# Kernel tuning notes

Measured on AMD Instinct MI355X. Metric: run time of the kernel, lower is better.

Reference implementation:

```python
import jax, jax.numpy as jnp
import numpy as np

_SAMPLING_EPS = 1e-05
_RMAX = 0.9999999403953552          # largest float32 uniform from tl.rand
_RMAX_LOG = -5.960464477539063e-08  # log(_RMAX)


def setup_inputs() -> dict:
    key = jax.random.key(0)
    k1, k2, k3, k4, k5 = jax.random.split(key, 5)
    B, V = 256, 128000
    logits = jax.random.normal(k1, (B, V), dtype=jnp.float32) * 4.0
    temperature = jax.random.uniform(k2, (B,), dtype=jnp.float32, minval=0.1, maxval=1.5)
    top_k = jax.random.randint(k3, (B,), 1, 1000).astype(jnp.int32)
    top_p = jax.random.uniform(k4, (B,), dtype=jnp.float32, minval=0.5, maxval=1.0)
    gumbel_u = jax.random.uniform(k5, (B, V), dtype=jnp.float32)
    return {
        "logits": logits,
        "temperature": temperature,
        "top_k": top_k,
        "top_p": top_p,
        "gumbel_u": gumbel_u,
        "num_logprobs": 20,
    }


def reference(logits, temperature, top_k, top_p, gumbel_u, num_logprobs):
    B, V = logits.shape
    # --- apply_temperature: divide by temp, temp<eps treated as 1.0 (greedy) ---
    temp = jnp.where(temperature < _SAMPLING_EPS, 1.0, temperature)
    logits = logits.astype(jnp.float32) / temp[:, None]

    # --- apply_top_k_top_p: sort ascending, mask, scatter back ---
    idx_sort = jnp.argsort(logits, axis=-1)                      # ascending
    logits_sort = jnp.take_along_axis(logits, idx_sort, axis=-1)
    # top-k: value of the k-th largest is at position V-k in ascending order
    k_pos = (V - top_k.astype(jnp.int32))[:, None]
    thresh = jnp.take_along_axis(logits_sort, k_pos, axis=-1)    # [B,1]
    logits_sort = jnp.where(logits_sort < thresh, -jnp.inf, logits_sort)
    # top-p: drop ascending prefix whose cumulative prob <= 1-p (keep last)
    probs_sort = jax.nn.softmax(logits_sort, axis=-1)
    cum = jnp.cumsum(probs_sort, axis=-1)
    mask_p = cum <= (1.0 - top_p)[:, None]
    mask_p = mask_p.at[:, -1].set(False)
    logits_sort = jnp.where(mask_p, -jnp.inf, logits_sort)
    # unsort back to vocab order
    inv = jnp.argsort(idx_sort, axis=-1)
    logits_f = jnp.take_along_axis(logits_sort, inv, axis=-1)

    # --- softmax + gumbel-trick sampling: argmax(p / -log(u)) ---
    probs = jax.nn.softmax(logits_f, axis=-1)
    q = -jnp.where(gumbel_u >= _RMAX, _RMAX_LOG, jnp.log(gumbel_u))
    greedy = (temperature < _SAMPLING_EPS)[:, None]  # kernel skips these rows
    ratio = jnp.where(greedy, probs, probs / q)
    sampled = jnp.argmax(ratio, axis=-1)             # [B]

    # --- gather_logprobs ---
    logprobs = jax.nn.log_softmax(logits_f, axis=-1)
    sampled_lp = jnp.take_along_axis(logprobs, sampled[:, None], axis=-1)  # [B,1]
    ranks = jnp.sum(logprobs > sampled_lp, axis=-1)                        # [B]
    topk_lp, topk_idx = jax.lax.top_k(logprobs, num_logprobs)
    indices = jnp.concatenate([sampled[:, None], topk_idx], axis=1)        # [B,1+K]
    lp_vals = jnp.concatenate([sampled_lp, topk_lp], axis=1)               # [B,1+K]

    return sampled[:, None], indices, lp_vals, ranks
```

## Files before the change

### kernel.cpp

```cpp
#include <hip/hip_runtime.h>
#include <math.h>

#define NTHR 1024
#define CAP 4096
#define BINS 4096

#define RMAX_F 0.9999999403953552f
#define RMAX_LOG_F -5.960464477539063e-08f
#define NEG_BIG -3.0e38f

__device__ __forceinline__ unsigned keyOf(float v) {
    unsigned b = __float_as_uint(v);
    return (b & 0x80000000u) ? ~b : (b | 0x80000000u);
}
__device__ __forceinline__ float valOfKey(unsigned k) {
    unsigned b = (k & 0x80000000u) ? (k ^ 0x80000000u) : ~k;
    return __uint_as_float(b);
}

__global__ __launch_bounds__(NTHR) void sampler_kernel(
    const float* __restrict__ logits,
    const float* __restrict__ temperature,
    const int* __restrict__ top_kv,
    const float* __restrict__ top_pv,
    const float* __restrict__ gumbel,
    float* __restrict__ out,
    int B, int V, int K)
{
    const int r = blockIdx.x;
    const int tid = threadIdx.x;
    const int lane = tid & 63;

    __shared__ unsigned long long cand[CAP];
    __shared__ int scanI[NTHR];
    __shared__ float varr[1024];
    __shared__ float Earr[1024];
    __shared__ float sfx[1024];
    __shared__ unsigned char flagArr[1024];
    __shared__ unsigned bitmap[64];
    __shared__ unsigned s_prefix;
    __shared__ int s_cntgt, s_total, s_lvl;
    __shared__ int s_ncand, s_nkeep, s_rank, s_g0, s_g1;
    __shared__ unsigned long long s_amax;
    __shared__ float s_vs;

    unsigned* hist = (unsigned*)cand;

    const float* row = logits + (long long)r * V;
    const float* urow = gumbel + (long long)r * V;

    float traw = temperature[r];
    bool greedy = traw < 1e-5f;
    float t = greedy ? 1.0f : traw;
    int k = top_kv[r];
    if (k < 1) k = 1;
    if (k > V) k = V;
    float p = top_pv[r];

    const float4* row4 = (const float4*)row;
    const int V4 = V >> 2;
    const int Vt = V4 << 2;
    const unsigned cpy = tid & 1u;

    for (int i = tid; i < BINS * 2; i += NTHR) hist[i] = 0;
    __syncthreads();
    for (int i = tid; i < V4; i += NTHR) {
        float4 l4 = row4[i];
        unsigned k0 = keyOf(l4.x), k1 = keyOf(l4.y), k2 = keyOf(l4.z), k3 = keyOf(l4.w);
        atomicAdd(&hist[((k0 >> 20) << 1) | cpy], 1u);
        atomicAdd(&hist[((k1 >> 20) << 1) | cpy], 1u);
        atomicAdd(&hist[((k2 >> 20) << 1) | cpy], 1u);
        atomicAdd(&hist[((k3 >> 20) << 1) | cpy], 1u);
    }
    for (int i = Vt + tid; i < V; i += NTHR) {
        unsigned key = keyOf(row[i]);
        atomicAdd(&hist[((key >> 20) << 1) | cpy], 1u);
    }
    __syncthreads();
    {
        int base = tid << 2;
        int cs = 0;
        #pragma unroll
        for (int j = 0; j < 4; ++j)
            cs += (int)(hist[(base + j) * 2] + hist[(base + j) * 2 + 1]);
        scanI[tid] = cs;
    }
    __syncthreads();
    for (int d = 1; d < NTHR; d <<= 1) {
        int v = (tid + d < NTHR) ? scanI[tid + d] : 0;
        __syncthreads();
        scanI[tid] += v;
        __syncthreads();
    }
    {
        int mine = scanI[tid];
        int above = (tid + 1 < NTHR) ? scanI[tid + 1] : 0;
        if (mine >= k && above < k) {
            int base = tid << 2;
            int run = above;
            for (int b = base + 3; b >= base; --b) {
                int mb = (int)(hist[b * 2] + hist[b * 2 + 1]);
                if (run + mb >= k) {
                    s_prefix = (unsigned)b; s_cntgt = run; s_total = run + mb; s_lvl = 0;
                    break;
                }
                run += mb;
            }
        }
    }
    for (int level = 1; level <= 2; ++level) {
        __syncthreads();
        if (s_total <= CAP) break;
        for (int i = tid; i < 512; i += NTHR) hist[i] = 0;
        __syncthreads();
        unsigned pfx = s_prefix;
        const int msh = 32 - (12 + 8 * (level - 1));
        const int bsh = msh - 8;
        for (int i = tid; i < V4; i += NTHR) {
            float4 l4 = row4[i];
            float vv[4] = { l4.x, l4.y, l4.z, l4.w };
            #pragma unroll
            for (int j = 0; j < 4; ++j) {
                unsigned key = keyOf(vv[j]);
                if ((key >> msh) == pfx)
                    atomicAdd(&hist[(((key >> bsh) & 255u) << 1) | cpy], 1u);
            }
        }
        for (int i = Vt + tid; i < V; i += NTHR) {
            unsigned key = keyOf(row[i]);
            if ((key >> msh) == pfx)
                atomicAdd(&hist[(((key >> bsh) & 255u) << 1) | cpy], 1u);
        }
        __syncthreads();
        if (tid == 0) {
            int run = s_cntgt;
            for (int b = 255; b >= 0; --b) {
                int mb = (int)(hist[b * 2] + hist[b * 2 + 1]);
                if (run + mb >= k) {
                    s_prefix = (pfx << 8) | (unsigned)b; s_cntgt = run; s_total = run + mb;
                    break;
                }
                run += mb;
            }
            s_lvl = level;
        }
    }
    __syncthreads();
    const unsigned tlo = s_prefix << (20 - 8 * s_lvl);
    if (tid == 0) s_ncand = 0;
    __syncthreads();

    for (int i = tid; i < V4; i += NTHR) {
        float4 l4 = row4[i];
        float vv[4] = { l4.x, l4.y, l4.z, l4.w };
        #pragma unroll
        for (int j = 0; j < 4; ++j) {
            unsigned key = keyOf(vv[j]);
            bool pred = (key >= tlo);
            unsigned long long mask = __ballot(pred ? 1 : 0);
            if (mask) {
                int leader = __ffsll(mask) - 1;
                int cnt = __popcll(mask);
                int base = 0;
                if (lane == leader) base = atomicAdd(&s_ncand, cnt);
                base = __shfl(base, leader);
                if (pred) {
                    int pos = base + __popcll(mask & ((1ULL << lane) - 1ULL));
                    if (pos < CAP) {
                        unsigned gidx = (unsigned)(i * 4 + j);
                        cand[pos] = ((unsigned long long)key << 32) | (unsigned)(~gidx);
                    }
                }
            }
        }
    }
    for (int i = Vt + tid; i < V; i += NTHR) {
        unsigned key = keyOf(row[i]);
        bool pred = (key >= tlo);
        unsigned long long mask = __ballot(pred ? 1 : 0);
        if (mask) {
            int leader = __ffsll(mask) - 1;
            int cnt = __popcll(mask);
            int base = 0;
            if (lane == leader) base = atomicAdd(&s_ncand, cnt);
            base = __shfl(base, leader);
            if (pred) {
                int pos = base + __popcll(mask & ((1ULL << lane) - 1ULL));
                if (pos < CAP) {
                    unsigned gidx = (unsigned)i;
                    cand[pos] = ((unsigned long long)key << 32) | (unsigned)(~gidx);
                }
            }
        }
    }
    __syncthreads();
    int ncand = s_ncand; if (ncand > CAP) ncand = CAP;
    if (k > ncand) k = ncand;

    int P = 2; while (P < ncand) P <<= 1;
    for (int i = ncand + tid; i < P; i += NTHR) cand[i] = 0ULL;
    __syncthreads();
    for (int size = 2; size <= P; size <<= 1) {
        for (int stride = size >> 1; stride > 0; stride >>= 1) {
            for (int i = tid; i < P; i += NTHR) {
                int j = i ^ stride;
                if (j > i) {
                    unsigned long long a = cand[i], b = cand[j];
                    bool up = ((i & size) == 0);
                    bool sw = up ? (a < b) : (a > b);
                    if (sw) { cand[i] = b; cand[j] = a; }
                }
            }
            __syncthreads();
        }
    }

    for (int i = tid; i < 1024; i += NTHR)
        varr[i] = (i < ncand) ? (valOfKey((unsigned)(cand[i] >> 32)) / t) : NEG_BIG;
    __syncthreads();

    const float m = varr[0];
    const float tkeyV = varr[k - 1];
    int ntop = k;
    while (ntop < ncand) {
        float vi = (ntop < 1024) ? varr[ntop]
                                 : (valOfKey((unsigned)(cand[ntop] >> 32)) / t);
        if (vi != tkeyV) break;
        ++ntop;
    }
    if (ntop > 1024) ntop = 1024;

    for (int i = tid; i < 1024; i += NTHR) {
        float e = (i < ntop) ? expf(varr[i] - m) : 0.0f;
        Earr[i] = e;
        sfx[i] = e;
    }
    __syncthreads();
    for (int d = 1; d < 1024; d <<= 1) {
        float t0 = (tid + d < 1024) ? sfx[tid + d] : 0.0f;
        __syncthreads();
        sfx[tid] += t0;
        __syncthreads();
    }
    const float Zp = sfx[0];
    const float cmp = 1.0f - p;
    if (tid == 0) { s_nkeep = 0; s_rank = 0; s_amax = 0ULL; }
    for (int i = tid; i < 64; i += NTHR) bitmap[i] = 0;
    __syncthreads();
    {
        int local = 0;
        for (int i = tid; i < ntop; i += NTHR)
            if (sfx[i] / Zp > cmp) local++;
        if (local) atomicAdd(&s_nkeep, local);
    }
    __syncthreads();
    const int nkeep = s_nkeep;
    if (tid == 0) {
        float vb = varr[nkeep - 1];
        int g0 = nkeep - 1;
        while (g0 > 0 && varr[g0 - 1] == vb) --g0;
        int g1 = nkeep;
        while (g1 < ntop && varr[g1] == vb) ++g1;
        s_g0 = g0; s_g1 = g1;
    }
    __syncthreads();
    const int g0 = s_g0, g1 = s_g1;
    const int mkeep = nkeep - g0;
    for (int i = g0 + tid; i < g1; i += NTHR) {
        unsigned gi = ~(unsigned)(cand[i] & 0xFFFFFFFFull);
        int rk = 0;
        for (int j = g0; j < g1; ++j) {
            unsigned gj = ~(unsigned)(cand[j] & 0xFFFFFFFFull);
            if (gj > gi) rk++;
        }
        flagArr[i] = (rk < mkeep) ? 1 : 0;
    }
    __syncthreads();

    const float Z2 = (nkeep < 1024) ? (Zp - sfx[nkeep]) : Zp;
    const float L = logf(Z2);

    for (int i = tid; i < g1; i += NTHR) {
        if (i < g0 || flagArr[i]) {
            unsigned lo = (unsigned)(cand[i] & 0xFFFFFFFFull);
            unsigned gidx = ~lo;
            float u = urow[gidx];
            float q = -((u >= RMAX_F) ? RMAX_LOG_F : logf(u));
            float prob = Earr[i] / Z2;
            float ratio = greedy ? prob : (prob / q);
            unsigned long long comp = ((unsigned long long)__float_as_uint(ratio) << 32) | lo;
            atomicMax(&s_amax, comp);
            if (gidx < 2048) atomicOr(&bitmap[gidx >> 5], 1u << (gidx & 31));
        }
    }
    __syncthreads();
    const unsigned samp_lo = (unsigned)(s_amax & 0xFFFFFFFFull);
    const unsigned samp = ~samp_lo;
    for (int i = tid; i < ntop; i += NTHR)
        if ((unsigned)(cand[i] & 0xFFFFFFFFull) == samp_lo) s_vs = varr[i];
    __syncthreads();
    const float lp_s = (s_vs - m) - L;
    {
        int local = 0;
        for (int i = tid; i < nkeep; i += NTHR)
            if ((varr[i] - m) - L > lp_s) local++;
        if (local) atomicAdd(&s_rank, local);
    }
    __syncthreads();

    if (tid == 0) {
        float* o_samp = out;
        float* o_idx  = out + B;
        float* o_lp   = out + B + (long long)B * (K + 1);
        float* o_rank = out + B + 2LL * B * (K + 1);
        long long rowo = (long long)r * (K + 1);

        o_samp[r] = (float)samp;
        o_idx[rowo] = (float)samp;
        o_lp[rowo] = lp_s;
        o_rank[r] = (float)s_rank;

        int ntk = (nkeep < K) ? nkeep : K;
        int slot = 0, i = 0;
        while (slot < ntk && i < g1) {
            float v = varr[i];
            int re = i + 1;
            while (re < g1 && varr[re] == v) ++re;
            long long last = -1;
            while (slot < ntk) {
                unsigned best = 0xFFFFFFFFu;
                for (int j = i; j < re; ++j) {
                    if (j >= g0 && !flagArr[j]) continue;
                    unsigned gj = ~(unsigned)(cand[j] & 0xFFFFFFFFull);
                    if ((long long)gj > last && gj < best) best = gj;
                }
                if (best == 0xFFFFFFFFu) break;
                o_idx[rowo + 1 + slot] = (float)best;
                o_lp[rowo + 1 + slot] = (v - m) - L;
                last = best; ++slot;
            }
            i = re;
        }
        if (nkeep < K) {
            int j = 0;
            for (int c = nkeep; c < K; ++c) {
                while (bitmap[j >> 5] & (1u << (j & 31))) ++j;
                o_idx[rowo + 1 + c] = (float)j;
                o_lp[rowo + 1 + c] = NEG_BIG;
                ++j;
            }
        }
    }
}

extern "C" void kernel_launch(void* const* d_in, const int* in_sizes, int n_in,
                              void* d_out, int out_size, void* d_ws, size_t ws_size,
                              hipStream_t stream) {
    const float* logits      = (const float*)d_in[0];
    const float* temperature = (const float*)d_in[1];
    const int*   top_k       = (const int*)d_in[2];
    const float* top_p       = (const float*)d_in[3];
    const float* gumbel      = (const float*)d_in[4];
    int B = in_sizes[1];
    int V = in_sizes[0] / B;
    int K = (out_size / B - 4) / 2;
    sampler_kernel<<<B, NTHR, 0, stream>>>(logits, temperature, top_k, top_p,
                                           gumbel, (float*)d_out, B, V, K);
}
```

Measured before the change: 317.1 us.

## Refine candidate threshold, register bitonic sort, warp-level scans and reductions

Unrolls the histogram and candidate-collection passes to issue four float4 loads per iteration. Replaces the shared-memory Hillis-Steele scan with wave shuffle scans. When more than 1024 candidates survive, a refinement histogram over the candidates narrows the threshold so the sort runs in registers with shuffles for strides below 64. Argmax, keep-count and rank reductions now use wave shuffles before the shared atomics, and the serial top-K output loop on thread 0 is replaced by parallel per-thread slot computation. The changes add code complexity, and the guard-band refinement is a risk for threshold-tie correctness.

```diff
diff --git a/kernel.cpp b/kernel.cpp
--- a/kernel.cpp
+++ b/kernel.cpp
@@ -4,6 +4,8 @@
 #define NTHR 1024
 #define CAP 4096
 #define BINS 4096
+#define SMALL 1024
+#define GUARD 16u
 
 #define RMAX_F 0.9999999403953552f
 #define RMAX_LOG_F -5.960464477539063e-08f
@@ -16,6 +18,11 @@
 __device__ __forceinline__ float valOfKey(unsigned k) {
     unsigned b = (k & 0x80000000u) ? (k ^ 0x80000000u) : ~k;
     return __uint_as_float(b);
+}
+__device__ __forceinline__ unsigned long long shflXor64(unsigned long long v, int m) {
+    int lo = __shfl_xor((int)(unsigned)v, m);
+    int hi = __shfl_xor((int)(unsigned)(v >> 32), m);
+    return ((unsigned long long)(unsigned)hi << 32) | (unsigned)lo;
 }
 
 __global__ __launch_bounds__(NTHR) void sampler_kernel(
@@ -30,9 +37,12 @@
     const int r = blockIdx.x;
     const int tid = threadIdx.x;
     const int lane = tid & 63;
+    const int wid = tid >> 6;
 
     __shared__ unsigned long long cand[CAP];
-    __shared__ int scanI[NTHR];
+    __shared__ unsigned long long cand2[SMALL];
+    __shared__ unsigned refHist[512];
+    __shared__ int wtotI[16];
     __shared__ float varr[1024];
     __shared__ float Earr[1024];
     __shared__ float sfx[1024];
@@ -40,7 +50,7 @@
     __shared__ unsigned bitmap[64];
     __shared__ unsigned s_prefix;
     __shared__ int s_cntgt, s_total, s_lvl;
-    __shared__ int s_ncand, s_nkeep, s_rank, s_g0, s_g1;
+    __shared__ int s_ncand, s_nc2, s_nkeep, s_rank, s_g0, s_g1;
     __shared__ unsigned long long s_amax;
     __shared__ float s_vs;
 
@@ -64,17 +74,27 @@
 
     for (int i = tid; i < BINS * 2; i += NTHR) hist[i] = 0;
     __syncthreads();
-    for (int i = tid; i < V4; i += NTHR) {
-        float4 l4 = row4[i];
-        unsigned k0 = keyOf(l4.x), k1 = keyOf(l4.y), k2 = keyOf(l4.z), k3 = keyOf(l4.w);
-        atomicAdd(&hist[((k0 >> 20) << 1) | cpy], 1u);
-        atomicAdd(&hist[((k1 >> 20) << 1) | cpy], 1u);
-        atomicAdd(&hist[((k2 >> 20) << 1) | cpy], 1u);
-        atomicAdd(&hist[((k3 >> 20) << 1) | cpy], 1u);
-    }
-    for (int i = Vt + tid; i < V; i += NTHR) {
-        unsigned key = keyOf(row[i]);
-        atomicAdd(&hist[((key >> 20) << 1) | cpy], 1u);
+#define H4(v4) do { \
+        atomicAdd(&hist[((keyOf((v4).x) >> 20) << 1) | cpy], 1u); \
+        atomicAdd(&hist[((keyOf((v4).y) >> 20) << 1) | cpy], 1u); \
+        atomicAdd(&hist[((keyOf((v4).z) >> 20) << 1) | cpy], 1u); \
+        atomicAdd(&hist[((keyOf((v4).w) >> 20) << 1) | cpy], 1u); \
+    } while (0)
+    {
+        int i = tid;
+        for (; i + 3 * NTHR < V4; i += 4 * NTHR) {
+            float4 a = row4[i];
+            float4 b = row4[i + NTHR];
+            float4 c = row4[i + 2 * NTHR];
+            float4 d = row4[i + 3 * NTHR];
+            H4(a); H4(b); H4(c); H4(d);
+        }
+        for (; i < V4; i += NTHR) {
+            float4 a = row4[i];
+            H4(a);
+        }
+        for (int ii = Vt + tid; ii < V; ii += NTHR)
+            atomicAdd(&hist[((keyOf(row[ii]) >> 20) << 1) | cpy], 1u);
     }
     __syncthreads();
     {
@@ -83,20 +103,19 @@
         #pragma unroll
         for (int j = 0; j < 4; ++j)
             cs += (int)(hist[(base + j) * 2] + hist[(base + j) * 2 + 1]);
-        scanI[tid] = cs;
-    }
-    __syncthreads();
-    for (int d = 1; d < NTHR; d <<= 1) {
-        int v = (tid + d < NTHR) ? scanI[tid + d] : 0;
-        __syncthreads();
-        scanI[tid] += v;
-        __syncthreads();
-    }
-    {
-        int mine = scanI[tid];
-        int above = (tid + 1 < NTHR) ? scanI[tid + 1] : 0;
+        int vv = cs;
+        #pragma unroll
+        for (int d = 1; d < 64; d <<= 1) {
+            int o = __shfl_down(vv, d);
+            if (lane + d < 64) vv += o;
+        }
+        if (lane == 0) wtotI[wid] = vv;
+        __syncthreads();
+        int off = 0;
+        for (int w = wid + 1; w < 16; ++w) off += wtotI[w];
+        int mine = vv + off;
+        int above = mine - cs;
         if (mine >= k && above < k) {
-            int base = tid << 2;
             int run = above;
             for (int b = base + 3; b >= base; --b) {
                 int mb = (int)(hist[b * 2] + hist[b * 2 + 1]);
@@ -147,77 +166,173 @@
     }
     __syncthreads();
     const unsigned tlo = s_prefix << (20 - 8 * s_lvl);
+    const float thrF = valOfKey(tlo);
     if (tid == 0) s_ncand = 0;
     __syncthreads();
 
-    for (int i = tid; i < V4; i += NTHR) {
-        float4 l4 = row4[i];
-        float vv[4] = { l4.x, l4.y, l4.z, l4.w };
-        #pragma unroll
-        for (int j = 0; j < 4; ++j) {
-            unsigned key = keyOf(vv[j]);
-            bool pred = (key >= tlo);
+#define EMIT_CAND(val, gidx_) do { \
+        bool pred = ((val) >= thrF); \
+        unsigned long long mask = __ballot(pred ? 1 : 0); \
+        if (mask) { \
+            int leader = __ffsll(mask) - 1; \
+            int cnt = __popcll(mask); \
+            int bpos = 0; \
+            if (lane == leader) bpos = atomicAdd(&s_ncand, cnt); \
+            bpos = __shfl(bpos, leader); \
+            if (pred) { \
+                int pos = bpos + __popcll(mask & ((1ULL << lane) - 1ULL)); \
+                if (pos < CAP) { \
+                    unsigned key = keyOf(val); \
+                    cand[pos] = ((unsigned long long)key << 32) | (unsigned)(~(gidx_)); \
+                } \
+            } \
+        } \
+    } while (0)
+#define C4(v4, i4) do { \
+        EMIT_CAND((v4).x, (unsigned)((i4) * 4 + 0)); \
+        EMIT_CAND((v4).y, (unsigned)((i4) * 4 + 1)); \
+        EMIT_CAND((v4).z, (unsigned)((i4) * 4 + 2)); \
+        EMIT_CAND((v4).w, (unsigned)((i4) * 4 + 3)); \
+    } while (0)
+    {
+        int i = tid;
+        for (; i + 3 * NTHR < V4; i += 4 * NTHR) {
+            float4 a = row4[i];
+            float4 b = row4[i + NTHR];
+            float4 c = row4[i + 2 * NTHR];
+            float4 d = row4[i + 3 * NTHR];
+            C4(a, i); C4(b, i + NTHR); C4(c, i + 2 * NTHR); C4(d, i + 3 * NTHR);
+        }
+        for (; i < V4; i += NTHR) {
+            float4 a = row4[i];
+            C4(a, i);
+        }
+        for (int ii = Vt + tid; ii < V; ii += NTHR) {
+            float lv = row[ii];
+            EMIT_CAND(lv, (unsigned)ii);
+        }
+    }
+    __syncthreads();
+    int ncand = s_ncand; if (ncand > CAP) ncand = CAP;
+    if (k > ncand) k = ncand;
+
+    bool fromC2 = false;
+    bool bigSort = false;
+    if (ncand > SMALL) {
+        unsigned pfx = s_prefix;
+        int run = s_cntgt;
+        int bb = 20 - 8 * s_lvl;
+        while (bb > 0) {
+            int step = (bb >= 8) ? 8 : bb;
+            bb -= step;
+            int nbins = 1 << step;
+            for (int i = tid; i < nbins * 2; i += NTHR) refHist[i] = 0;
+            __syncthreads();
+            for (int i = tid; i < ncand; i += NTHR) {
+                unsigned key = (unsigned)(cand[i] >> 32);
+                if ((key >> (bb + step)) == pfx)
+                    atomicAdd(&refHist[(((key >> bb) & (unsigned)(nbins - 1)) << 1) | cpy], 1u);
+            }
+            __syncthreads();
+            int cnt = 0;
+            if (tid < 256) cnt = (tid < nbins) ? (int)(refHist[tid * 2] + refHist[tid * 2 + 1]) : 0;
+            int vv = cnt;
+            #pragma unroll
+            for (int d = 1; d < 64; d <<= 1) {
+                int o = __shfl_down(vv, d);
+                if (lane + d < 64) vv += o;
+            }
+            if (tid < 256 && lane == 0) wtotI[wid] = vv;
+            __syncthreads();
+            if (tid < 256) {
+                int off = 0;
+                for (int w = wid + 1; w < 4; ++w) off += wtotI[w];
+                int incl = vv + off;
+                int abv = incl - cnt;
+                int kk = k - run;
+                if (incl >= kk && abv < kk) {
+                    s_prefix = (pfx << step) | (unsigned)tid;
+                    s_cntgt = run + abv;
+                }
+            }
+            __syncthreads();
+            pfx = s_prefix;
+            run = s_cntgt;
+        }
+        unsigned tref = (pfx >= tlo + GUARD) ? (pfx - GUARD) : tlo;
+        if (tid == 0) s_nc2 = 0;
+        __syncthreads();
+        for (int i = tid; i < ncand; i += NTHR) {
+            unsigned long long cv = cand[i];
+            bool pred = ((unsigned)(cv >> 32) >= tref);
             unsigned long long mask = __ballot(pred ? 1 : 0);
             if (mask) {
                 int leader = __ffsll(mask) - 1;
-                int cnt = __popcll(mask);
-                int base = 0;
-                if (lane == leader) base = atomicAdd(&s_ncand, cnt);
-                base = __shfl(base, leader);
+                int cnt2 = __popcll(mask);
+                int bpos = 0;
+                if (lane == leader) bpos = atomicAdd(&s_nc2, cnt2);
+                bpos = __shfl(bpos, leader);
                 if (pred) {
-                    int pos = base + __popcll(mask & ((1ULL << lane) - 1ULL));
-                    if (pos < CAP) {
-                        unsigned gidx = (unsigned)(i * 4 + j);
-                        cand[pos] = ((unsigned long long)key << 32) | (unsigned)(~gidx);
+                    int pos = bpos + __popcll(mask & ((1ULL << lane) - 1ULL));
+                    if (pos < SMALL) cand2[pos] = cv;
+                }
+            }
+        }
+        __syncthreads();
+        int nc2 = s_nc2;
+        if (nc2 <= SMALL) { ncand = nc2; fromC2 = true; }
+        else bigSort = true;
+    }
+
+    unsigned long long vreg = 0ULL;
+    if (!bigSort) {
+        const unsigned long long* src = fromC2 ? cand2 : cand;
+        unsigned long long v = (tid < ncand) ? src[tid] : 0ULL;
+        #pragma unroll
+        for (int size = 2; size <= SMALL; size <<= 1) {
+            #pragma unroll
+            for (int stride = size >> 1; stride > 0; stride >>= 1) {
+                unsigned long long o;
+                if (stride < 64) {
+                    o = shflXor64(v, stride);
+                } else {
+                    cand[tid] = v;
+                    __syncthreads();
+                    o = cand[tid ^ stride];
+                    __syncthreads();
+                }
+                bool takeMax = (((tid & size) == 0) == ((tid & stride) == 0));
+                unsigned long long mx = (v > o) ? v : o;
+                unsigned long long mn = (v > o) ? o : v;
+                v = takeMax ? mx : mn;
+            }
+        }
+        cand[tid] = v;
+        vreg = v;
+        varr[tid] = (tid < ncand) ? (valOfKey((unsigned)(vreg >> 32)) / t) : NEG_BIG;
+        __syncthreads();
+    } else {
+        int P = 2; while (P < ncand) P <<= 1;
+        for (int i = ncand + tid; i < P; i += NTHR) cand[i] = 0ULL;
+        __syncthreads();
+        for (int size = 2; size <= P; size <<= 1) {
+            for (int stride = size >> 1; stride > 0; stride >>= 1) {
+                for (int i = tid; i < P; i += NTHR) {
+                    int j = i ^ stride;
+                    if (j > i) {
+                        unsigned long long a = cand[i], b = cand[j];
+                        bool up = ((i & size) == 0);
+                        bool sw = up ? (a < b) : (a > b);
+                        if (sw) { cand[i] = b; cand[j] = a; }
                     }
                 }
-            }
-        }
-    }
-    for (int i = Vt + tid; i < V; i += NTHR) {
-        unsigned key = keyOf(row[i]);
-        bool pred = (key >= tlo);
-        unsigned long long mask = __ballot(pred ? 1 : 0);
-        if (mask) {
-            int leader = __ffsll(mask) - 1;
-            int cnt = __popcll(mask);
-            int base = 0;
-            if (lane == leader) base = atomicAdd(&s_ncand, cnt);
-            base = __shfl(base, leader);
-            if (pred) {
-                int pos = base + __popcll(mask & ((1ULL << lane) - 1ULL));
-                if (pos < CAP) {
-                    unsigned gidx = (unsigned)i;
-                    cand[pos] = ((unsigned long long)key << 32) | (unsigned)(~gidx);
-                }
-            }
-        }
-    }
-    __syncthreads();
-    int ncand = s_ncand; if (ncand > CAP) ncand = CAP;
-    if (k > ncand) k = ncand;
-
-    int P = 2; while (P < ncand) P <<= 1;
-    for (int i = ncand + tid; i < P; i += NTHR) cand[i] = 0ULL;
-    __syncthreads();
-    for (int size = 2; size <= P; size <<= 1) {
-        for (int stride = size >> 1; stride > 0; stride >>= 1) {
-            for (int i = tid; i < P; i += NTHR) {
-                int j = i ^ stride;
-                if (j > i) {
-                    unsigned long long a = cand[i], b = cand[j];
-                    bool up = ((i & size) == 0);
-                    bool sw = up ? (a < b) : (a > b);
-                    if (sw) { cand[i] = b; cand[j] = a; }
-                }
-            }
-            __syncthreads();
-        }
-    }
-
-    for (int i = tid; i < 1024; i += NTHR)
-        varr[i] = (i < ncand) ? (valOfKey((unsigned)(cand[i] >> 32)) / t) : NEG_BIG;
-    __syncthreads();
+                __syncthreads();
+            }
+        }
+        for (int i = tid; i < 1024; i += NTHR)
+            varr[i] = (i < ncand) ? (valOfKey((unsigned)(cand[i] >> 32)) / t) : NEG_BIG;
+        __syncthreads();
+    }
 
     const float m = varr[0];
     const float tkeyV = varr[k - 1];
@@ -230,10 +345,10 @@
     }
     if (ntop > 1024) ntop = 1024;
 
-    for (int i = tid; i < 1024; i += NTHR) {
-        float e = (i < ntop) ? expf(varr[i] - m) : 0.0f;
-        Earr[i] = e;
-        sfx[i] = e;
+    {
+        float e = (tid < ntop) ? expf(varr[tid] - m) : 0.0f;
+        Earr[tid] = e;
+        sfx[tid] = e;
     }
     __syncthreads();
     for (int d = 1; d < 1024; d <<= 1) {
@@ -251,7 +366,9 @@
         int local = 0;
         for (int i = tid; i < ntop; i += NTHR)
             if (sfx[i] / Zp > cmp) local++;
-        if (local) atomicAdd(&s_nkeep, local);
+        #pragma unroll
+        for (int d = 1; d < 64; d <<= 1) local += __shfl_xor(local, d);
+        if (lane == 0 && local) atomicAdd(&s_nkeep, local);
     }
     __syncthreads();
     const int nkeep = s_nkeep;
@@ -280,18 +397,27 @@
     const float Z2 = (nkeep < 1024) ? (Zp - sfx[nkeep]) : Zp;
     const float L = logf(Z2);
 
-    for (int i = tid; i < g1; i += NTHR) {
-        if (i < g0 || flagArr[i]) {
-            unsigned lo = (unsigned)(cand[i] & 0xFFFFFFFFull);
-            unsigned gidx = ~lo;
-            float u = urow[gidx];
-            float q = -((u >= RMAX_F) ? RMAX_LOG_F : logf(u));
-            float prob = Earr[i] / Z2;
-            float ratio = greedy ? prob : (prob / q);
-            unsigned long long comp = ((unsigned long long)__float_as_uint(ratio) << 32) | lo;
-            atomicMax(&s_amax, comp);
-            if (gidx < 2048) atomicOr(&bitmap[gidx >> 5], 1u << (gidx & 31));
-        }
+    {
+        unsigned long long lm = 0ULL;
+        for (int i = tid; i < g1; i += NTHR) {
+            if (i < g0 || flagArr[i]) {
+                unsigned lo = (unsigned)(cand[i] & 0xFFFFFFFFull);
+                unsigned gidx = ~lo;
+                float u = urow[gidx];
+                float q = -((u >= RMAX_F) ? RMAX_LOG_F : logf(u));
+                float prob = Earr[i] / Z2;
+                float ratio = greedy ? prob : (prob / q);
+                unsigned long long comp = ((unsigned long long)__float_as_uint(ratio) << 32) | lo;
+                if (comp > lm) lm = comp;
+                if (gidx < 2048) atomicOr(&bitmap[gidx >> 5], 1u << (gidx & 31));
+            }
+        }
+        #pragma unroll
+        for (int d = 1; d < 64; d <<= 1) {
+            unsigned long long o = shflXor64(lm, d);
+            if (o > lm) lm = o;
+        }
+        if (lane == 0 && lm) atomicMax(&s_amax, lm);
     }
     __syncthreads();
     const unsigned samp_lo = (unsigned)(s_amax & 0xFFFFFFFFull);
@@ -304,43 +430,54 @@
         int local = 0;
         for (int i = tid; i < nkeep; i += NTHR)
             if ((varr[i] - m) - L > lp_s) local++;
-        if (local) atomicAdd(&s_rank, local);
-    }
-    __syncthreads();
+        #pragma unroll
+        for (int d = 1; d < 64; d <<= 1) local += __shfl_xor(local, d);
+        if (lane == 0 && local) atomicAdd(&s_rank, local);
+    }
+    __syncthreads();
+
+    float* o_samp = out;
+    float* o_idx  = out + B;
+    float* o_lp   = out + B + (long long)B * (K + 1);
+    float* o_rank = out + B + 2LL * B * (K + 1);
+    const long long rowo = (long long)r * (K + 1);
+    const int ntk = (nkeep < K) ? nkeep : K;
+
+    if (tid < g1) {
+        const int i = tid;
+        bool kept = (i < g0) || flagArr[i];
+        if (kept) {
+            float v = varr[i];
+            int rs, re, base;
+            if (i >= g0) { rs = g0; re = g1; base = g0; }
+            else {
+                rs = i; while (rs > 0 && varr[rs - 1] == v) --rs;
+                re = i + 1; while (re < g1 && varr[re] == v) ++re;
+                base = rs;
+            }
+            if (base < ntk) {
+                unsigned myidx = ~(unsigned)(cand[i] & 0xFFFFFFFFull);
+                int cnt = 0;
+                for (int j = rs; j < re; ++j) {
+                    if (j == i) continue;
+                    if (j >= g0 && !flagArr[j]) continue;
+                    unsigned gj = ~(unsigned)(cand[j] & 0xFFFFFFFFull);
+                    if (gj < myidx) cnt++;
+                }
+                int slot = base + cnt;
+                if (slot < ntk) {
+                    o_idx[rowo + 1 + slot] = (float)myidx;
+                    o_lp[rowo + 1 + slot] = (v - m) - L;
+                }
+            }
+        }
+    }
 
     if (tid == 0) {
-        float* o_samp = out;
-        float* o_idx  = out + B;
-        float* o_lp   = out + B + (long long)B * (K + 1);
-        float* o_rank = out + B + 2LL * B * (K + 1);
-        long long rowo = (long long)r * (K + 1);
-
         o_samp[r] = (float)samp;
         o_idx[rowo] = (float)samp;
         o_lp[rowo] = lp_s;
         o_rank[r] = (float)s_rank;
-
-        int ntk = (nkeep < K) ? nkeep : K;
-        int slot = 0, i = 0;
-        while (slot < ntk && i < g1) {
-            float v = varr[i];
-            int re = i + 1;
-            while (re < g1 && varr[re] == v) ++re;
-            long long last = -1;
-            while (slot < ntk) {
-                unsigned best = 0xFFFFFFFFu;
-                for (int j = i; j < re; ++j) {
-                    if (j >= g0 && !flagArr[j]) continue;
-                    unsigned gj = ~(unsigned)(cand[j] & 0xFFFFFFFFull);
-                    if ((long long)gj > last && gj < best) best = gj;
-                }
-                if (best == 0xFFFFFFFFu) break;
-                o_idx[rowo + 1 + slot] = (float)best;
-                o_lp[rowo + 1 + slot] = (v - m) - L;
-                last = best; ++slot;
-            }
-            i = re;
-        }
         if (nkeep < K) {
             int j = 0;
             for (int c = nkeep; c < K; ++c) {
```

Result: faster. 281.2 us (-11.3%).
